# Kernel tuning notes

Hardware: AMD Instinct MI355X
Metric: run time of the kernel (lower is better)

Reference implementation:

```python
import jax, jax.numpy as jnp
import numpy as np

PATCH = 15  # box-filter kernel size (odd -> SAME padding == padding=PATCH//2, stride 1)


def _box_filter(x, k):
    """All-ones kxk conv2d, stride 1, zero pad k//2. x: (N,1,H,W).
    The ones kernel is separable: ones(k,k) = ones(k,1) @ ones(1,k)."""
    dn = ('NCHW', 'OIHW', 'NCHW')
    kh = jnp.ones((1, 1, k, 1), x.dtype)
    kw = jnp.ones((1, 1, 1, k), x.dtype)
    x = jax.lax.conv_general_dilated(x, kh, (1, 1), 'SAME', dimension_numbers=dn)
    x = jax.lax.conv_general_dilated(x, kw, (1, 1), 'SAME', dimension_numbers=dn)
    return x


def _rgb_to_yuv420(rgb):
    """rgb: (N,3,H,W) -> y:(N,H,W), u,v:(N,H/2,W/2) (2x2 avg-pooled chroma)."""
    r, g, b = rgb[:, 0], rgb[:, 1], rgb[:, 2]
    y = 0.299 * r + 0.587 * g + 0.114 * b
    u = -0.169 * r - 0.331 * g + 0.5 * b + 128.0
    v = 0.5 * r - 0.46 * g - 0.04 * b + 128.0
    n, h, w = u.shape
    u = u.reshape(n, h // 2, 2, w // 2, 2).mean(axis=(2, 4))
    v = v.reshape(n, h // 2, 2, w // 2, 2).mean(axis=(2, 4))
    return y, u, v


def _filtered_channels(img, k):
    y, u, v = _rgb_to_yuv420(img)
    return (_box_filter(y[:, None], k),
            _box_filter(u[:, None], k),
            _box_filter(v[:, None], k))


def setup_inputs() -> dict:
    key = jax.random.key(0)
    k1, k2 = jax.random.split(key)
    input_ = jax.random.uniform(k1, (16, 3, 512, 512), dtype=jnp.float32)
    target = jax.random.uniform(k2, (16, 3, 512, 512), dtype=jnp.float32)
    return {"input": input_, "target": target}


def reference(input, target):
    yi, ui, vi = _filtered_channels(input, PATCH)
    yt, ut, vt = _filtered_channels(target, PATCH)
    mse = lambda a, b: jnp.mean((a - b) ** 2)
    return mse(yi, yt) + mse(ui, ut) + mse(vi, vt)
```

## Files before the change

### kernel.cpp

```cpp
#include <hip/hip_runtime.h>

#define NIMG 16
#define H 512
#define W 512
#define CH 256
#define CW 256
#define HALF 7

static __device__ __forceinline__ unsigned short f2bf(float f) {
    unsigned u = __float_as_uint(f);
    u += 0x7FFFu + ((u >> 16) & 1u);
    return (unsigned short)(u >> 16);
}
static __device__ __forceinline__ float bf2f(unsigned short h) {
    return __uint_as_float(((unsigned)h) << 16);
}
static __device__ __forceinline__ float bflo(unsigned v) {
    return __uint_as_float(v << 16);
}
static __device__ __forceinline__ float bfhi(unsigned v) {
    return __uint_as_float(v & 0xFFFF0000u);
}

__global__ void diff_hbox_kernel(const float* __restrict__ in, const float* __restrict__ tgt,
                                 unsigned short* __restrict__ hY,
                                 unsigned short* __restrict__ hUV) {
    __shared__ float sY0[W + 16], sY1[W + 16], sU[CW + 16], sV[CW + 16];
    const int tid = threadIdx.x;
    const int cy = blockIdx.x & (CH - 1);
    const int n  = blockIdx.x >> 8;

    if (tid < 8) {
        sY0[tid] = 0.f; sY0[W + 8 + tid] = 0.f;
        sY1[tid] = 0.f; sY1[W + 8 + tid] = 0.f;
        sU[tid] = 0.f;  sU[CW + 8 + tid] = 0.f;
        sV[tid] = 0.f;  sV[CW + 8 + tid] = 0.f;
    }

    const size_t plane = (size_t)H * W;
    const float* pi = in  + (size_t)n * 3 * plane;
    const float* pt = tgt + (size_t)n * 3 * plane;

    const int y0 = cy << 1;
    const int x0 = tid << 1;
    const size_t o0 = (size_t)y0 * W + x0;
    const size_t o1 = o0 + W;

    float2 ir0 = *(const float2*)(pi + o0);
    float2 ir1 = *(const float2*)(pi + o1);
    float2 ig0 = *(const float2*)(pi + plane + o0);
    float2 ig1 = *(const float2*)(pi + plane + o1);
    float2 ib0 = *(const float2*)(pi + 2 * plane + o0);
    float2 ib1 = *(const float2*)(pi + 2 * plane + o1);

    float2 tr0 = *(const float2*)(pt + o0);
    float2 tr1 = *(const float2*)(pt + o1);
    float2 tg0 = *(const float2*)(pt + plane + o0);
    float2 tg1 = *(const float2*)(pt + plane + o1);
    float2 tb0 = *(const float2*)(pt + 2 * plane + o0);
    float2 tb1 = *(const float2*)(pt + 2 * plane + o1);

    float dr00 = ir0.x - tr0.x, dr01 = ir0.y - tr0.y;
    float dr10 = ir1.x - tr1.x, dr11 = ir1.y - tr1.y;
    float dg00 = ig0.x - tg0.x, dg01 = ig0.y - tg0.y;
    float dg10 = ig1.x - tg1.x, dg11 = ig1.y - tg1.y;
    float db00 = ib0.x - tb0.x, db01 = ib0.y - tb0.y;
    float db10 = ib1.x - tb1.x, db11 = ib1.y - tb1.y;

    sY0[8 + x0]     = 0.299f * dr00 + 0.587f * dg00 + 0.114f * db00;
    sY0[8 + x0 + 1] = 0.299f * dr01 + 0.587f * dg01 + 0.114f * db01;
    sY1[8 + x0]     = 0.299f * dr10 + 0.587f * dg10 + 0.114f * db10;
    sY1[8 + x0 + 1] = 0.299f * dr11 + 0.587f * dg11 + 0.114f * db11;

    float sr = dr00 + dr01 + dr10 + dr11;
    float sg = dg00 + dg01 + dg10 + dg11;
    float sb = db00 + db01 + db10 + db11;
    sU[8 + tid] = (-0.169f * sr - 0.331f * sg + 0.5f * sb) * 0.25f;
    sV[8 + tid] = ( 0.5f   * sr - 0.46f  * sg - 0.04f * sb) * 0.25f;

    __syncthreads();

    {
        const int row = tid >> 7;
        const int xb  = (tid & 127) << 2;
        const float* srow = row ? sY1 : sY0;
        float s = 0.f;
#pragma unroll
        for (int j = 1; j <= 15; ++j) s += srow[xb + j];
        ushort4 o;
        o.x = f2bf(s); s += srow[xb + 16] - srow[xb + 1];
        o.y = f2bf(s); s += srow[xb + 17] - srow[xb + 2];
        o.z = f2bf(s); s += srow[xb + 18] - srow[xb + 3];
        o.w = f2bf(s);
        *(ushort4*)(hY + ((size_t)n * H + y0 + row) * W + xb) = o;
    }

    {
        const int uv = tid >> 7;
        const int t  = tid & 127;
        const int xb = t << 1;
        const float* srow = uv ? sV : sU;
        float s = 0.f;
#pragma unroll
        for (int j = 1; j <= 15; ++j) s += srow[xb + j];
        ushort2 o;
        o.x = f2bf(s); s += srow[xb + 16] - srow[xb + 1];
        o.y = f2bf(s);
        const size_t p = (size_t)(n * 2 + uv);
        *(ushort2*)(hUV + (p * CH + cy) * CW + xb) = o;
    }
}

#define K2_NBLK 3072
__global__ void vbox_sq_partial_kernel(const unsigned short* __restrict__ hY,
                                       const unsigned short* __restrict__ hUV,
                                       float invY, float invC,
                                       float* __restrict__ partials) {
    const int b = blockIdx.x;
    float s0 = 0.f, s1 = 0.f, s2 = 0.f, s3 = 0.f;
    float s4 = 0.f, s5 = 0.f, s6 = 0.f, s7 = 0.f;
    float inv;
    if (b < 2048) {
        const int q  = b * 256 + threadIdx.x;
        const int x8 = q & 63;
        const int y  = (q >> 6) & (H - 1);
        const int img = q >> 15;
        const unsigned short* col = hY + ((size_t)img << 18) + (x8 << 3);
#pragma unroll
        for (int t = -HALF; t <= HALF; ++t) {
            const int yy = y + t;
            const int yc = min(max(yy, 0), H - 1);
            const uint4 v = *(const uint4*)(col + ((size_t)yc << 9));
            const float m = (yy == yc) ? 1.f : 0.f;
            s0 += m * bflo(v.x); s1 += m * bfhi(v.x);
            s2 += m * bflo(v.y); s3 += m * bfhi(v.y);
            s4 += m * bflo(v.z); s5 += m * bfhi(v.z);
            s6 += m * bflo(v.w); s7 += m * bfhi(v.w);
        }
        inv = invY;
    } else {
        const int q  = (b - 2048) * 256 + threadIdx.x;
        const int x8 = q & 31;
        const int y  = (q >> 5) & (CH - 1);
        const int plane = q >> 13;
        const unsigned short* col = hUV + ((size_t)plane << 16) + (x8 << 3);
#pragma unroll
        for (int t = -HALF; t <= HALF; ++t) {
            const int yy = y + t;
            const int yc = min(max(yy, 0), CH - 1);
            const uint4 v = *(const uint4*)(col + ((size_t)yc << 8));
            const float m = (yy == yc) ? 1.f : 0.f;
            s0 += m * bflo(v.x); s1 += m * bfhi(v.x);
            s2 += m * bflo(v.y); s3 += m * bfhi(v.y);
            s4 += m * bflo(v.z); s5 += m * bfhi(v.z);
            s6 += m * bflo(v.w); s7 += m * bfhi(v.w);
        }
        inv = invC;
    }
    float val = ((s0 * s0 + s1 * s1) + (s2 * s2 + s3 * s3) +
                 (s4 * s4 + s5 * s5) + (s6 * s6 + s7 * s7)) * inv;

    for (int o = 32; o > 0; o >>= 1) val += __shfl_down(val, o, 64);
    __shared__ float part[4];
    const int lane = threadIdx.x & 63, wid = threadIdx.x >> 6;
    if (lane == 0) part[wid] = val;
    __syncthreads();
    if (threadIdx.x == 0)
        partials[b] = part[0] + part[1] + part[2] + part[3];
}

__global__ void final_reduce_kernel(const float* __restrict__ partials, int n,
                                    float* __restrict__ out) {
    float s = 0.f;
    for (int i = threadIdx.x; i < n; i += 256) s += partials[i];
    for (int o = 32; o > 0; o >>= 1) s += __shfl_down(s, o, 64);
    __shared__ float part[4];
    const int lane = threadIdx.x & 63, wid = threadIdx.x >> 6;
    if (lane == 0) part[wid] = s;
    __syncthreads();
    if (threadIdx.x == 0)
        *out = part[0] + part[1] + part[2] + part[3];
}

extern "C" void kernel_launch(void* const* d_in, const int* in_sizes, int n_in,
                              void* d_out, int out_size, void* d_ws, size_t ws_size,
                              hipStream_t stream) {
    const float* input  = (const float*)d_in[0];
    const float* target = (const float*)d_in[1];
    float* out = (float*)d_out;

    const size_t yElems = (size_t)NIMG * H * W;
    const size_t cElems = (size_t)NIMG * CH * CW;

    unsigned short* hY  = (unsigned short*)d_ws;
    unsigned short* hUV = hY + yElems;
    float* partials = (float*)(hUV + 2 * cElems);

    diff_hbox_kernel<<<NIMG * CH, 256, 0, stream>>>(input, target, hY, hUV);

    vbox_sq_partial_kernel<<<K2_NBLK, 256, 0, stream>>>(
        hY, hUV, 1.0f / (float)yElems, 1.0f / (float)cElems, partials);

    final_reduce_kernel<<<1, 256, 0, stream>>>(partials, K2_NBLK, out);
}
```

Before: 129.4 us.

## Fuse horizontal and vertical box filters into one tiled shared-memory kernel

Replaces the two-pass pipeline, which wrote bf16 horizontally filtered planes to global memory and read them back, with a single kernel per 64x256 output tile. Each tile loads a haloed region of input and target into LDS, runs a vertical sliding-window sum in place, then a horizontal sliding window in registers, and accumulates squared sums into per-block partials. This removes the intermediate global round trip and one launch. In exchange it recomputes halo pixels, launches only 256 blocks of 512 threads with large LDS, and keeps chroma in bf16 in LDS.

```diff
diff --git a/kernel.cpp b/kernel.cpp
--- a/kernel.cpp
+++ b/kernel.cpp
@@ -3,9 +3,16 @@
 #define NIMG 16
 #define H 512
 #define W 512
-#define CH 256
-#define CW 256
 #define HALF 7
+
+#define RT 64
+#define CT 256
+#define YROWS 78
+#define YCOLS 272
+#define YSTR 276
+#define CROWS 46
+#define CCOLS 142
+#define CSTR 152
 
 static __device__ __forceinline__ unsigned short f2bf(float f) {
     unsigned u = __float_as_uint(f);
@@ -22,151 +29,166 @@
     return __uint_as_float(v & 0xFFFF0000u);
 }
 
-__global__ void diff_hbox_kernel(const float* __restrict__ in, const float* __restrict__ tgt,
-                                 unsigned short* __restrict__ hY,
-                                 unsigned short* __restrict__ hUV) {
-    __shared__ float sY0[W + 16], sY1[W + 16], sU[CW + 16], sV[CW + 16];
+__global__ __launch_bounds__(512) void fused_loss_kernel(
+        const float* __restrict__ in, const float* __restrict__ tgt,
+        float invY, float invC, float* __restrict__ partials) {
+    __shared__ float sY[YROWS * YSTR];
+    __shared__ unsigned short sU[CROWS * CSTR];
+    __shared__ unsigned short sV[CROWS * CSTR];
+    __shared__ float part[8];
+
     const int tid = threadIdx.x;
-    const int cy = blockIdx.x & (CH - 1);
-    const int n  = blockIdx.x >> 8;
-
-    if (tid < 8) {
-        sY0[tid] = 0.f; sY0[W + 8 + tid] = 0.f;
-        sY1[tid] = 0.f; sY1[W + 8 + tid] = 0.f;
-        sU[tid] = 0.f;  sU[CW + 8 + tid] = 0.f;
-        sV[tid] = 0.f;  sV[CW + 8 + tid] = 0.f;
-    }
+    const int b = blockIdx.x;
+    const int n  = b >> 4;
+    const int rt = (b >> 1) & 7;
+    const int ct = b & 1;
+    const int r0 = rt << 6;
+    const int c0 = ct << 8;
 
     const size_t plane = (size_t)H * W;
     const float* pi = in  + (size_t)n * 3 * plane;
     const float* pt = tgt + (size_t)n * 3 * plane;
 
-    const int y0 = cy << 1;
-    const int x0 = tid << 1;
-    const size_t o0 = (size_t)y0 * W + x0;
-    const size_t o1 = o0 + W;
-
-    float2 ir0 = *(const float2*)(pi + o0);
-    float2 ir1 = *(const float2*)(pi + o1);
-    float2 ig0 = *(const float2*)(pi + plane + o0);
-    float2 ig1 = *(const float2*)(pi + plane + o1);
-    float2 ib0 = *(const float2*)(pi + 2 * plane + o0);
-    float2 ib1 = *(const float2*)(pi + 2 * plane + o1);
-
-    float2 tr0 = *(const float2*)(pt + o0);
-    float2 tr1 = *(const float2*)(pt + o1);
-    float2 tg0 = *(const float2*)(pt + plane + o0);
-    float2 tg1 = *(const float2*)(pt + plane + o1);
-    float2 tb0 = *(const float2*)(pt + 2 * plane + o0);
-    float2 tb1 = *(const float2*)(pt + 2 * plane + o1);
-
-    float dr00 = ir0.x - tr0.x, dr01 = ir0.y - tr0.y;
-    float dr10 = ir1.x - tr1.x, dr11 = ir1.y - tr1.y;
-    float dg00 = ig0.x - tg0.x, dg01 = ig0.y - tg0.y;
-    float dg10 = ig1.x - tg1.x, dg11 = ig1.y - tg1.y;
-    float db00 = ib0.x - tb0.x, db01 = ib0.y - tb0.y;
-    float db10 = ib1.x - tb1.x, db11 = ib1.y - tb1.y;
-
-    sY0[8 + x0]     = 0.299f * dr00 + 0.587f * dg00 + 0.114f * db00;
-    sY0[8 + x0 + 1] = 0.299f * dr01 + 0.587f * dg01 + 0.114f * db01;
-    sY1[8 + x0]     = 0.299f * dr10 + 0.587f * dg10 + 0.114f * db10;
-    sY1[8 + x0 + 1] = 0.299f * dr11 + 0.587f * dg11 + 0.114f * db11;
-
-    float sr = dr00 + dr01 + dr10 + dr11;
-    float sg = dg00 + dg01 + dg10 + dg11;
-    float sb = db00 + db01 + db10 + db11;
-    sU[8 + tid] = (-0.169f * sr - 0.331f * sg + 0.5f * sb) * 0.25f;
-    sV[8 + tid] = ( 0.5f   * sr - 0.46f  * sg - 0.04f * sb) * 0.25f;
-
-    __syncthreads();
+#pragma unroll 2
+    for (int i = tid; i < CROWS * 144; i += 512) {
+        const int pr = i / 144;
+        const int pc = i - pr * 144;
+        const int yy = r0 - 14 + 2 * pr;
+        const int xx = c0 - 14 + 2 * pc;
+
+        float dr00=0.f,dr01=0.f,dr10=0.f,dr11=0.f;
+        float dg00=0.f,dg01=0.f,dg10=0.f,dg11=0.f;
+        float db00=0.f,db01=0.f,db10=0.f,db11=0.f;
+
+        if ((unsigned)yy < H && (unsigned)xx < W && pc < CCOLS) {
+            const int off = yy * W + xx;
+            const float2 ir0 = *(const float2*)(pi + off);
+            const float2 ir1 = *(const float2*)(pi + off + W);
+            const float2 ig0 = *(const float2*)(pi + plane + off);
+            const float2 ig1 = *(const float2*)(pi + plane + off + W);
+            const float2 ib0 = *(const float2*)(pi + 2 * plane + off);
+            const float2 ib1 = *(const float2*)(pi + 2 * plane + off + W);
+            const float2 tr0 = *(const float2*)(pt + off);
+            const float2 tr1 = *(const float2*)(pt + off + W);
+            const float2 tg0 = *(const float2*)(pt + plane + off);
+            const float2 tg1 = *(const float2*)(pt + plane + off + W);
+            const float2 tb0 = *(const float2*)(pt + 2 * plane + off);
+            const float2 tb1 = *(const float2*)(pt + 2 * plane + off + W);
+            dr00 = ir0.x - tr0.x; dr01 = ir0.y - tr0.y;
+            dr10 = ir1.x - tr1.x; dr11 = ir1.y - tr1.y;
+            dg00 = ig0.x - tg0.x; dg01 = ig0.y - tg0.y;
+            dg10 = ig1.x - tg1.x; dg11 = ig1.y - tg1.y;
+            db00 = ib0.x - tb0.x; db01 = ib0.y - tb0.y;
+            db10 = ib1.x - tb1.x; db11 = ib1.y - tb1.y;
+        }
+
+        const float y00 = 0.299f * dr00 + 0.587f * dg00 + 0.114f * db00;
+        const float y01 = 0.299f * dr01 + 0.587f * dg01 + 0.114f * db01;
+        const float y10 = 0.299f * dr10 + 0.587f * dg10 + 0.114f * db10;
+        const float y11 = 0.299f * dr11 + 0.587f * dg11 + 0.114f * db11;
+
+        const int ly0 = 2 * pr - 7;
+        const int lx0 = 2 * pc - 6;
+        if ((unsigned)lx0 < YCOLS) {
+            if ((unsigned)ly0 < YROWS)
+                *(float2*)&sY[ly0 * YSTR + lx0] = make_float2(y00, y01);
+            if ((unsigned)(ly0 + 1) < YROWS)
+                *(float2*)&sY[(ly0 + 1) * YSTR + lx0] = make_float2(y10, y11);
+        }
+
+        const float sr = dr00 + dr01 + dr10 + dr11;
+        const float sg = dg00 + dg01 + dg10 + dg11;
+        const float sb = db00 + db01 + db10 + db11;
+        sU[pr * CSTR + pc] = f2bf((-0.169f * sr - 0.331f * sg + 0.5f  * sb) * 0.25f);
+        sV[pr * CSTR + pc] = f2bf(( 0.5f   * sr - 0.46f  * sg - 0.04f * sb) * 0.25f);
+    }
+    __syncthreads();
+
+    for (int t = tid; t < YCOLS + 2 * CCOLS; t += 512) {
+        if (t < YCOLS) {
+            const int j = t;
+            float s = 0.f;
+#pragma unroll
+            for (int r = 0; r < 14; ++r) s += sY[r * YSTR + j];
+#pragma unroll
+            for (int y = 0; y < RT; ++y) {
+                s += sY[(y + 14) * YSTR + j];
+                const float o = s;
+                s -= sY[y * YSTR + j];
+                sY[y * YSTR + j] = o;
+            }
+        } else {
+            const int jj = t - YCOLS;
+            unsigned short* sp = (jj < CCOLS) ? sU : sV;
+            const int j = (jj < CCOLS) ? jj : jj - CCOLS;
+            float s = 0.f;
+#pragma unroll
+            for (int r = 0; r < 14; ++r) s += bf2f(sp[r * CSTR + j]);
+#pragma unroll
+            for (int y = 0; y < RT / 2; ++y) {
+                s += bf2f(sp[(y + 14) * CSTR + j]);
+                const float o = s;
+                s -= bf2f(sp[y * CSTR + j]);
+                sp[y * CSTR + j] = f2bf(o);
+            }
+        }
+    }
+    __syncthreads();
+
+    float accY = 0.f, accC = 0.f;
+    const int wv = tid >> 6, lane = tid & 63;
 
     {
-        const int row = tid >> 7;
-        const int xb  = (tid & 127) << 2;
-        const float* srow = row ? sY1 : sY0;
+        float wn[48];
+        const int base = lane * YSTR + (wv << 5);
+#pragma unroll
+        for (int j = 0; j < 12; ++j)
+            *(float4*)&wn[4 * j] = *(const float4*)&sY[base + 4 * j];
         float s = 0.f;
 #pragma unroll
-        for (int j = 1; j <= 15; ++j) s += srow[xb + j];
-        ushort4 o;
-        o.x = f2bf(s); s += srow[xb + 16] - srow[xb + 1];
-        o.y = f2bf(s); s += srow[xb + 17] - srow[xb + 2];
-        o.z = f2bf(s); s += srow[xb + 18] - srow[xb + 3];
-        o.w = f2bf(s);
-        *(ushort4*)(hY + ((size_t)n * H + y0 + row) * W + xb) = o;
+        for (int j = 1; j <= 14; ++j) s += wn[j];
+#pragma unroll
+        for (int k = 0; k < 32; ++k) {
+            s += wn[15 + k];
+            accY += s * s;
+            s -= wn[1 + k];
+        }
     }
 
     {
-        const int uv = tid >> 7;
-        const int t  = tid & 127;
-        const int xb = t << 1;
-        const float* srow = uv ? sV : sU;
+        const int pl = lane >> 5, y = lane & 31;
+        const unsigned short* sp = pl ? sV : sU;
+        const int base = y * CSTR + (wv << 4);
+        float wn[32];
+#pragma unroll
+        for (int j = 0; j < 4; ++j) {
+            const uint4 v = *(const uint4*)&sp[base + 8 * j];
+            wn[8 * j + 0] = bflo(v.x); wn[8 * j + 1] = bfhi(v.x);
+            wn[8 * j + 2] = bflo(v.y); wn[8 * j + 3] = bfhi(v.y);
+            wn[8 * j + 4] = bflo(v.z); wn[8 * j + 5] = bfhi(v.z);
+            wn[8 * j + 6] = bflo(v.w); wn[8 * j + 7] = bfhi(v.w);
+        }
         float s = 0.f;
 #pragma unroll
-        for (int j = 1; j <= 15; ++j) s += srow[xb + j];
-        ushort2 o;
-        o.x = f2bf(s); s += srow[xb + 16] - srow[xb + 1];
-        o.y = f2bf(s);
-        const size_t p = (size_t)(n * 2 + uv);
-        *(ushort2*)(hUV + (p * CH + cy) * CW + xb) = o;
-    }
-}
-
-#define K2_NBLK 3072
-__global__ void vbox_sq_partial_kernel(const unsigned short* __restrict__ hY,
-                                       const unsigned short* __restrict__ hUV,
-                                       float invY, float invC,
-                                       float* __restrict__ partials) {
-    const int b = blockIdx.x;
-    float s0 = 0.f, s1 = 0.f, s2 = 0.f, s3 = 0.f;
-    float s4 = 0.f, s5 = 0.f, s6 = 0.f, s7 = 0.f;
-    float inv;
-    if (b < 2048) {
-        const int q  = b * 256 + threadIdx.x;
-        const int x8 = q & 63;
-        const int y  = (q >> 6) & (H - 1);
-        const int img = q >> 15;
-        const unsigned short* col = hY + ((size_t)img << 18) + (x8 << 3);
-#pragma unroll
-        for (int t = -HALF; t <= HALF; ++t) {
-            const int yy = y + t;
-            const int yc = min(max(yy, 0), H - 1);
-            const uint4 v = *(const uint4*)(col + ((size_t)yc << 9));
-            const float m = (yy == yc) ? 1.f : 0.f;
-            s0 += m * bflo(v.x); s1 += m * bfhi(v.x);
-            s2 += m * bflo(v.y); s3 += m * bfhi(v.y);
-            s4 += m * bflo(v.z); s5 += m * bfhi(v.z);
-            s6 += m * bflo(v.w); s7 += m * bfhi(v.w);
-        }
-        inv = invY;
-    } else {
-        const int q  = (b - 2048) * 256 + threadIdx.x;
-        const int x8 = q & 31;
-        const int y  = (q >> 5) & (CH - 1);
-        const int plane = q >> 13;
-        const unsigned short* col = hUV + ((size_t)plane << 16) + (x8 << 3);
-#pragma unroll
-        for (int t = -HALF; t <= HALF; ++t) {
-            const int yy = y + t;
-            const int yc = min(max(yy, 0), CH - 1);
-            const uint4 v = *(const uint4*)(col + ((size_t)yc << 8));
-            const float m = (yy == yc) ? 1.f : 0.f;
-            s0 += m * bflo(v.x); s1 += m * bfhi(v.x);
-            s2 += m * bflo(v.y); s3 += m * bfhi(v.y);
-            s4 += m * bflo(v.z); s5 += m * bfhi(v.z);
-            s6 += m * bflo(v.w); s7 += m * bfhi(v.w);
-        }
-        inv = invC;
-    }
-    float val = ((s0 * s0 + s1 * s1) + (s2 * s2 + s3 * s3) +
-                 (s4 * s4 + s5 * s5) + (s6 * s6 + s7 * s7)) * inv;
-
-    for (int o = 32; o > 0; o >>= 1) val += __shfl_down(val, o, 64);
-    __shared__ float part[4];
-    const int lane = threadIdx.x & 63, wid = threadIdx.x >> 6;
-    if (lane == 0) part[wid] = val;
-    __syncthreads();
-    if (threadIdx.x == 0)
-        partials[b] = part[0] + part[1] + part[2] + part[3];
+        for (int j = 0; j < 14; ++j) s += wn[j];
+#pragma unroll
+        for (int k = 0; k < 16; ++k) {
+            s += wn[14 + k];
+            accC += s * s;
+            s -= wn[k];
+        }
+    }
+
+    float v = accY * invY + accC * invC;
+    for (int o = 32; o > 0; o >>= 1) v += __shfl_down(v, o, 64);
+    if (lane == 0) part[wv] = v;
+    __syncthreads();
+    if (tid == 0) {
+        float s = 0.f;
+#pragma unroll
+        for (int j = 0; j < 8; ++j) s += part[j];
+        partials[b] = s;
+    }
 }
 
 __global__ void final_reduce_kernel(const float* __restrict__ partials, int n,
@@ -188,18 +210,11 @@
     const float* input  = (const float*)d_in[0];
     const float* target = (const float*)d_in[1];
     float* out = (float*)d_out;
-
-    const size_t yElems = (size_t)NIMG * H * W;
-    const size_t cElems = (size_t)NIMG * CH * CW;
-
-    unsigned short* hY  = (unsigned short*)d_ws;
-    unsigned short* hUV = hY + yElems;
-    float* partials = (float*)(hUV + 2 * cElems);
-
-    diff_hbox_kernel<<<NIMG * CH, 256, 0, stream>>>(input, target, hY, hUV);
-
-    vbox_sq_partial_kernel<<<K2_NBLK, 256, 0, stream>>>(
-        hY, hUV, 1.0f / (float)yElems, 1.0f / (float)cElems, partials);
-
-    final_reduce_kernel<<<1, 256, 0, stream>>>(partials, K2_NBLK, out);
-}
+    float* partials = (float*)d_ws;
+
+    const float invY = 1.0f / (float)((size_t)NIMG * H * W);
+    const float invC = 1.0f / (float)((size_t)NIMG * (H/2) * (W/2));
+
+    fused_loss_kernel<<<NIMG * 8 * 2, 512, 0, stream>>>(input, target, invY, invC, partials);
+    final_reduce_kernel<<<1, 256, 0, stream>>>(partials, NIMG * 8 * 2, out);
+}
```

Result: faster. 125.4 us (-3.1%).

## Fuse horizontal and vertical box filters into one streaming kernel with shared ring buffer

Applied to the files above, without the earlier changes.

Replaces the two-pass design (horizontal box to bf16 global scratch, then vertical box plus square reduction) with a single kernel per image band and column quarter. Each block streams row pairs, computes the YUV difference, runs horizontal sums into a shared-memory ring buffer, and keeps running vertical sums in registers. This removes the global intermediate round trip and the bf16 quantization. In exchange it uses few blocks, only 40 loader threads per step, and a sync per row step, so latency hiding is uncertain.

```diff
diff --git a/kernel.cpp b/kernel.cpp
--- a/kernel.cpp
+++ b/kernel.cpp
@@ -3,170 +3,164 @@
 #define NIMG 16
 #define H 512
 #define W 512
-#define CH 256
-#define CW 256
-#define HALF 7
 
-static __device__ __forceinline__ unsigned short f2bf(float f) {
-    unsigned u = __float_as_uint(f);
-    u += 0x7FFFu + ((u >> 16) & 1u);
-    return (unsigned short)(u >> 16);
-}
-static __device__ __forceinline__ float bf2f(unsigned short h) {
-    return __uint_as_float(((unsigned)h) << 16);
-}
-static __device__ __forceinline__ float bflo(unsigned v) {
-    return __uint_as_float(v << 16);
-}
-static __device__ __forceinline__ float bfhi(unsigned v) {
-    return __uint_as_float(v & 0xFFFF0000u);
-}
+#define DYW 148
+#define UVW 84
+#define HBYW 132
+#define HBCW 68
+#define NHBY 20
+#define NHBC 18
 
-__global__ void diff_hbox_kernel(const float* __restrict__ in, const float* __restrict__ tgt,
-                                 unsigned short* __restrict__ hY,
-                                 unsigned short* __restrict__ hUV) {
-    __shared__ float sY0[W + 16], sY1[W + 16], sU[CW + 16], sV[CW + 16];
+static __device__ __forceinline__ int wrap20(int x) { return x >= 20 ? x - 20 : x; }
+static __device__ __forceinline__ int wrap18(int x) { return x >= 18 ? x - 18 : x; }
+
+__global__ __launch_bounds__(256, 2) void fused_stream_kernel(
+        const float* __restrict__ in, const float* __restrict__ tgt,
+        float invY, float invC, float* __restrict__ partials) {
+    __shared__ float dYs[2][2][DYW];
+    __shared__ float dUVs[2][2][UVW];
+    __shared__ float hbY[NHBY][HBYW];
+    __shared__ float hbU[NHBC][HBCW];
+    __shared__ float hbV[NHBC][HBCW];
+    __shared__ float part[4];
+
     const int tid = threadIdx.x;
-    const int cy = blockIdx.x & (CH - 1);
-    const int n  = blockIdx.x >> 8;
-
-    if (tid < 8) {
-        sY0[tid] = 0.f; sY0[W + 8 + tid] = 0.f;
-        sY1[tid] = 0.f; sY1[W + 8 + tid] = 0.f;
-        sU[tid] = 0.f;  sU[CW + 8 + tid] = 0.f;
-        sV[tid] = 0.f;  sV[CW + 8 + tid] = 0.f;
-    }
+    const int b = blockIdx.x;
+    const int n     = b >> 5;
+    const int band  = (b >> 2) & 7;
+    const int quart = b & 3;
+    const int R0 = band << 6;
+    const int C0 = quart << 7;
+    const int P0 = band << 5;
 
     const size_t plane = (size_t)H * W;
     const float* pi = in  + (size_t)n * 3 * plane;
     const float* pt = tgt + (size_t)n * 3 * plane;
 
-    const int y0 = cy << 1;
-    const int x0 = tid << 1;
-    const size_t o0 = (size_t)y0 * W + x0;
-    const size_t o1 = o0 + W;
+    for (int i = tid; i < NHBY * HBYW; i += 256) (&hbY[0][0])[i] = 0.f;
+    for (int i = tid; i < NHBC * HBCW; i += 256) { (&hbU[0][0])[i] = 0.f; (&hbV[0][0])[i] = 0.f; }
 
-    float2 ir0 = *(const float2*)(pi + o0);
-    float2 ir1 = *(const float2*)(pi + o1);
-    float2 ig0 = *(const float2*)(pi + plane + o0);
-    float2 ig1 = *(const float2*)(pi + plane + o1);
-    float2 ib0 = *(const float2*)(pi + 2 * plane + o0);
-    float2 ib1 = *(const float2*)(pi + 2 * plane + o1);
+    const int cY  = tid & 127;
+    const int rp  = tid >> 7;
+    const int plc = (tid >> 6) & 1;
+    const int cC  = tid & 63;
+    float (*hbC)[HBCW] = plc ? hbV : hbU;
+    const bool isStageT = tid < 40;
+    const int xx = C0 - 16 + (tid << 2);
+    const bool cok = (unsigned)xx < W;
 
-    float2 tr0 = *(const float2*)(pt + o0);
-    float2 tr1 = *(const float2*)(pt + o1);
-    float2 tg0 = *(const float2*)(pt + plane + o0);
-    float2 tg1 = *(const float2*)(pt + plane + o1);
-    float2 tb0 = *(const float2*)(pt + 2 * plane + o0);
-    float2 tb1 = *(const float2*)(pt + 2 * plane + o1);
+    float sA = 0.f, sB = 0.f, sC = 0.f, accY = 0.f, accC = 0.f;
 
-    float dr00 = ir0.x - tr0.x, dr01 = ir0.y - tr0.y;
-    float dr10 = ir1.x - tr1.x, dr11 = ir1.y - tr1.y;
-    float dg00 = ig0.x - tg0.x, dg01 = ig0.y - tg0.y;
-    float dg10 = ig1.x - tg1.x, dg11 = ig1.y - tg1.y;
-    float db00 = ib0.x - tb0.x, db01 = ib0.y - tb0.y;
-    float db10 = ib1.x - tb1.x, db11 = ib1.y - tb1.y;
+    int slotW = (64 * band - 16) % 20; if (slotW < 0) slotW += 20;
+    int slotC = (32 * band - 8)  % 18; if (slotC < 0) slotC += 18;
 
-    sY0[8 + x0]     = 0.299f * dr00 + 0.587f * dg00 + 0.114f * db00;
-    sY0[8 + x0 + 1] = 0.299f * dr01 + 0.587f * dg01 + 0.114f * db01;
-    sY1[8 + x0]     = 0.299f * dr10 + 0.587f * dg10 + 0.114f * db10;
-    sY1[8 + x0 + 1] = 0.299f * dr11 + 0.587f * dg11 + 0.114f * db11;
+#pragma unroll 1
+    for (int s = -1; s <= 46; ++s) {
+        __syncthreads();
+        const int pcur = P0 - 7 + s;
 
-    float sr = dr00 + dr01 + dr10 + dr11;
-    float sg = dg00 + dg01 + dg10 + dg11;
-    float sb = db00 + db01 + db10 + db11;
-    sU[8 + tid] = (-0.169f * sr - 0.331f * sg + 0.5f * sb) * 0.25f;
-    sV[8 + tid] = ( 0.5f   * sr - 0.46f  * sg - 0.04f * sb) * 0.25f;
+        const float4 z4 = make_float4(0.f, 0.f, 0.f, 0.f);
+        float4 iRa=z4,iGa=z4,iBa=z4,tRa=z4,tGa=z4,tBa=z4;
+        float4 iRb=z4,iGb=z4,iBb=z4,tRb=z4,tGb=z4,tBb=z4;
+        const bool doStage = (s <= 44) && isStageT;
+        if (doStage && cok) {
+            const int pn = pcur + 1;
+            const int ra = 2 * pn, rb = 2 * pn + 1;
+            if ((unsigned)ra < H) {
+                const size_t o = (size_t)ra * W + xx;
+                iRa = *(const float4*)(pi + o);              tRa = *(const float4*)(pt + o);
+                iGa = *(const float4*)(pi + plane + o);      tGa = *(const float4*)(pt + plane + o);
+                iBa = *(const float4*)(pi + 2 * plane + o);  tBa = *(const float4*)(pt + 2 * plane + o);
+            }
+            if ((unsigned)rb < H) {
+                const size_t o = (size_t)rb * W + xx;
+                iRb = *(const float4*)(pi + o);              tRb = *(const float4*)(pt + o);
+                iGb = *(const float4*)(pi + plane + o);      tGb = *(const float4*)(pt + plane + o);
+                iBb = *(const float4*)(pi + 2 * plane + o);  tBb = *(const float4*)(pt + 2 * plane + o);
+            }
+        }
 
-    __syncthreads();
+        if (s >= 0 && s <= 45) {
+            const float* rowY = dYs[s & 1][rp];
+            const float t1 = (rowY[cY+1] + rowY[cY+2]) + (rowY[cY+3] + rowY[cY+4]);
+            const float t2 = (rowY[cY+5] + rowY[cY+6]) + (rowY[cY+7] + rowY[cY+8]);
+            const float t3 = (rowY[cY+9] + rowY[cY+10]) + (rowY[cY+11] + rowY[cY+12]);
+            const float t4 = (rowY[cY+13] + rowY[cY+14]) + rowY[cY+15];
+            hbY[wrap20(slotW + rp)][cY] = (t1 + t2) + (t3 + t4);
+            if (tid < 128) {
+                const float* rowC = dUVs[s & 1][plc];
+                const float u1 = (rowC[cC+1] + rowC[cC+2]) + (rowC[cC+3] + rowC[cC+4]);
+                const float u2 = (rowC[cC+5] + rowC[cC+6]) + (rowC[cC+7] + rowC[cC+8]);
+                const float u3 = (rowC[cC+9] + rowC[cC+10]) + (rowC[cC+11] + rowC[cC+12]);
+                const float u4 = (rowC[cC+13] + rowC[cC+14]) + rowC[cC+15];
+                hbC[slotC][cC] = (u1 + u2) + (u3 + u4);
+            }
+        }
 
-    {
-        const int row = tid >> 7;
-        const int xb  = (tid & 127) << 2;
-        const float* srow = row ? sY1 : sY0;
-        float s = 0.f;
-#pragma unroll
-        for (int j = 1; j <= 15; ++j) s += srow[xb + j];
-        ushort4 o;
-        o.x = f2bf(s); s += srow[xb + 16] - srow[xb + 1];
-        o.y = f2bf(s); s += srow[xb + 17] - srow[xb + 2];
-        o.z = f2bf(s); s += srow[xb + 18] - srow[xb + 3];
-        o.w = f2bf(s);
-        *(ushort4*)(hY + ((size_t)n * H + y0 + row) * W + xb) = o;
+        if (s >= 1) {
+            if (tid >= 128) {
+                const int k2 = wrap20(slotW + 2),  k3 = wrap20(slotW + 3),  k4 = wrap20(slotW + 4);
+                const int k17 = wrap20(slotW + 17), k18 = wrap20(slotW + 18), k19 = wrap20(slotW + 19);
+                const float h2 = hbY[k2][cY],  h3 = hbY[k3][cY],  h4 = hbY[k4][cY];
+                const float h17 = hbY[k17][cY], h18 = hbY[k18][cY], h19 = hbY[k19][cY];
+                sA += (h17 + h18) - (h2 + h3);
+                sB += (h18 + h19) - (h3 + h4);
+                const int yA = 2 * pcur - 9;
+                if ((unsigned)(yA - R0) < 64u)     accY += sA * sA;
+                if ((unsigned)(yA + 1 - R0) < 64u) accY += sB * sB;
+            } else {
+                const int kN = wrap18(slotC + 17), kO = wrap18(slotC + 2);
+                sC += hbC[kN][cC] - hbC[kO][cC];
+                if ((unsigned)(pcur - 8 - P0) < 32u) accC += sC * sC;
+            }
+        }
+
+        if (doStage) {
+            const float4 dRa = make_float4(iRa.x-tRa.x, iRa.y-tRa.y, iRa.z-tRa.z, iRa.w-tRa.w);
+            const float4 dGa = make_float4(iGa.x-tGa.x, iGa.y-tGa.y, iGa.z-tGa.z, iGa.w-tGa.w);
+            const float4 dBa = make_float4(iBa.x-tBa.x, iBa.y-tBa.y, iBa.z-tBa.z, iBa.w-tBa.w);
+            const float4 dRb = make_float4(iRb.x-tRb.x, iRb.y-tRb.y, iRb.z-tRb.z, iRb.w-tRb.w);
+            const float4 dGb = make_float4(iGb.x-tGb.x, iGb.y-tGb.y, iGb.z-tGb.z, iGb.w-tGb.w);
+            const float4 dBb = make_float4(iBb.x-tBb.x, iBb.y-tBb.y, iBb.z-tBb.z, iBb.w-tBb.w);
+            const int wb = (s + 1) & 1;
+            if (tid >= 2 && tid < 38) {
+                float4 ya, yb;
+                ya.x = 0.299f*dRa.x + 0.587f*dGa.x + 0.114f*dBa.x;
+                ya.y = 0.299f*dRa.y + 0.587f*dGa.y + 0.114f*dBa.y;
+                ya.z = 0.299f*dRa.z + 0.587f*dGa.z + 0.114f*dBa.z;
+                ya.w = 0.299f*dRa.w + 0.587f*dGa.w + 0.114f*dBa.w;
+                yb.x = 0.299f*dRb.x + 0.587f*dGb.x + 0.114f*dBb.x;
+                yb.y = 0.299f*dRb.y + 0.587f*dGb.y + 0.114f*dBb.y;
+                yb.z = 0.299f*dRb.z + 0.587f*dGb.z + 0.114f*dBb.z;
+                yb.w = 0.299f*dRb.w + 0.587f*dGb.w + 0.114f*dBb.w;
+                *(float4*)&dYs[wb][0][4 * tid - 8] = ya;
+                *(float4*)&dYs[wb][1][4 * tid - 8] = yb;
+            }
+            const float sr0 = (dRa.x + dRa.y) + (dRb.x + dRb.y);
+            const float sg0 = (dGa.x + dGa.y) + (dGb.x + dGb.y);
+            const float sb0 = (dBa.x + dBa.y) + (dBb.x + dBb.y);
+            const float sr1 = (dRa.z + dRa.w) + (dRb.z + dRb.w);
+            const float sg1 = (dGa.z + dGa.w) + (dGb.z + dGb.w);
+            const float sb1 = (dBa.z + dBa.w) + (dBb.z + dBb.w);
+            const float u0 = (-0.169f*sr0 - 0.331f*sg0 + 0.5f *sb0) * 0.25f;
+            const float u1 = (-0.169f*sr1 - 0.331f*sg1 + 0.5f *sb1) * 0.25f;
+            const float v0 = ( 0.5f  *sr0 - 0.46f *sg0 - 0.04f*sb0) * 0.25f;
+            const float v1 = ( 0.5f  *sr1 - 0.46f *sg1 - 0.04f*sb1) * 0.25f;
+            *(float2*)&dUVs[wb][0][2 * tid] = make_float2(u0, u1);
+            *(float2*)&dUVs[wb][1][2 * tid] = make_float2(v0, v1);
+        }
+
+        slotW = wrap20(slotW + 2);
+        slotC = wrap18(slotC + 1);
     }
 
-    {
-        const int uv = tid >> 7;
-        const int t  = tid & 127;
-        const int xb = t << 1;
-        const float* srow = uv ? sV : sU;
-        float s = 0.f;
-#pragma unroll
-        for (int j = 1; j <= 15; ++j) s += srow[xb + j];
-        ushort2 o;
-        o.x = f2bf(s); s += srow[xb + 16] - srow[xb + 1];
-        o.y = f2bf(s);
-        const size_t p = (size_t)(n * 2 + uv);
-        *(ushort2*)(hUV + (p * CH + cy) * CW + xb) = o;
-    }
-}
-
-#define K2_NBLK 3072
-__global__ void vbox_sq_partial_kernel(const unsigned short* __restrict__ hY,
-                                       const unsigned short* __restrict__ hUV,
-                                       float invY, float invC,
-                                       float* __restrict__ partials) {
-    const int b = blockIdx.x;
-    float s0 = 0.f, s1 = 0.f, s2 = 0.f, s3 = 0.f;
-    float s4 = 0.f, s5 = 0.f, s6 = 0.f, s7 = 0.f;
-    float inv;
-    if (b < 2048) {
-        const int q  = b * 256 + threadIdx.x;
-        const int x8 = q & 63;
-        const int y  = (q >> 6) & (H - 1);
-        const int img = q >> 15;
-        const unsigned short* col = hY + ((size_t)img << 18) + (x8 << 3);
-#pragma unroll
-        for (int t = -HALF; t <= HALF; ++t) {
-            const int yy = y + t;
-            const int yc = min(max(yy, 0), H - 1);
-            const uint4 v = *(const uint4*)(col + ((size_t)yc << 9));
-            const float m = (yy == yc) ? 1.f : 0.f;
-            s0 += m * bflo(v.x); s1 += m * bfhi(v.x);
-            s2 += m * bflo(v.y); s3 += m * bfhi(v.y);
-            s4 += m * bflo(v.z); s5 += m * bfhi(v.z);
-            s6 += m * bflo(v.w); s7 += m * bfhi(v.w);
-        }
-        inv = invY;
-    } else {
-        const int q  = (b - 2048) * 256 + threadIdx.x;
-        const int x8 = q & 31;
-        const int y  = (q >> 5) & (CH - 1);
-        const int plane = q >> 13;
-        const unsigned short* col = hUV + ((size_t)plane << 16) + (x8 << 3);
-#pragma unroll
-        for (int t = -HALF; t <= HALF; ++t) {
-            const int yy = y + t;
-            const int yc = min(max(yy, 0), CH - 1);
-            const uint4 v = *(const uint4*)(col + ((size_t)yc << 8));
-            const float m = (yy == yc) ? 1.f : 0.f;
-            s0 += m * bflo(v.x); s1 += m * bfhi(v.x);
-            s2 += m * bflo(v.y); s3 += m * bfhi(v.y);
-            s4 += m * bflo(v.z); s5 += m * bfhi(v.z);
-            s6 += m * bflo(v.w); s7 += m * bfhi(v.w);
-        }
-        inv = invC;
-    }
-    float val = ((s0 * s0 + s1 * s1) + (s2 * s2 + s3 * s3) +
-                 (s4 * s4 + s5 * s5) + (s6 * s6 + s7 * s7)) * inv;
-
-    for (int o = 32; o > 0; o >>= 1) val += __shfl_down(val, o, 64);
-    __shared__ float part[4];
-    const int lane = threadIdx.x & 63, wid = threadIdx.x >> 6;
-    if (lane == 0) part[wid] = val;
+    float v = accY * invY + accC * invC;
+    for (int o = 32; o > 0; o >>= 1) v += __shfl_down(v, o, 64);
+    const int lane = tid & 63, wv = tid >> 6;
+    if (lane == 0) part[wv] = v;
     __syncthreads();
-    if (threadIdx.x == 0)
-        partials[b] = part[0] + part[1] + part[2] + part[3];
+    if (tid == 0)
+        partials[b] = (part[0] + part[1]) + (part[2] + part[3]);
 }
 
 __global__ void final_reduce_kernel(const float* __restrict__ partials, int n,
@@ -188,18 +182,11 @@
     const float* input  = (const float*)d_in[0];
     const float* target = (const float*)d_in[1];
     float* out = (float*)d_out;
+    float* partials = (float*)d_ws;
 
-    const size_t yElems = (size_t)NIMG * H * W;
-    const size_t cElems = (size_t)NIMG * CH * CW;
+    const float invY = 1.0f / (float)((size_t)NIMG * H * W);
+    const float invC = 1.0f / (float)((size_t)NIMG * (H/2) * (W/2));
 
-    unsigned short* hY  = (unsigned short*)d_ws;
-    unsigned short* hUV = hY + yElems;
-    float* partials = (float*)(hUV + 2 * cElems);
-
-    diff_hbox_kernel<<<NIMG * CH, 256, 0, stream>>>(input, target, hY, hUV);
-
-    vbox_sq_partial_kernel<<<K2_NBLK, 256, 0, stream>>>(
-        hY, hUV, 1.0f / (float)yElems, 1.0f / (float)cElems, partials);
-
-    final_reduce_kernel<<<1, 256, 0, stream>>>(partials, K2_NBLK, out);
+    fused_stream_kernel<<<NIMG * 8 * 4, 256, 0, stream>>>(input, target, invY, invC, partials);
+    final_reduce_kernel<<<1, 256, 0, stream>>>(partials, NIMG * 8 * 4, out);
 }
```

Result: slower. 191.7 us (+48.2%).
